# Kernel tuning notes

Hardware: AMD Instinct MI355X
Metric: run time of the kernel (lower is better)

Reference implementation:

```python
import jax, jax.numpy as jnp
import numpy as np

E, K, CAP = 6, 2, 192
ALPHA, LOAD_PEN, MIN_USE, TEMP = 0.7, 2.0, 0.05, 1.0
BN_EPS = 1e-5
NEG = -1e30


def conv3x3(x, w, b=None):
    y = jax.lax.conv_general_dilated(x, w, (1, 1), 'SAME',
                                     dimension_numbers=('NCHW', 'OIHW', 'NCHW'))
    if b is not None:
        y = y + b[None, :, None, None]
    return y


def bn_eval(x, g, b):
    # fresh BatchNorm buffers: running_mean=0, running_var=1
    s = g / jnp.sqrt(1.0 + BN_EPS)
    return x * s[None, :, None, None] + b[None, :, None, None]


def maxpool2(x):
    return jax.lax.reduce_window(x, -jnp.inf, jax.lax.max,
                                 (1, 1, 2, 2), (1, 1, 2, 2), 'VALID')


def avgpool_to2(x):
    B, C, H, W = x.shape
    return x.reshape(B, C, 2, H // 2, 2, W // 2).mean(axis=(3, 5))


def expert_forward(p, x):
    h = jax.nn.relu(bn_eval(conv3x3(x, p['c1w'], p['c1b']), p['b1g'], p['b1b']))
    h = maxpool2(h)  # 32 -> 16
    h = jax.nn.relu(bn_eval(conv3x3(h, p['c2w'], p['c2b']), p['b2g'], p['b2b']))
    h = jax.nn.relu(bn_eval(conv3x3(h, p['c3w'], p['c3b']), p['b3g'], p['b3b']))
    h = maxpool2(h)  # 16 -> 8
    h = jax.nn.relu(bn_eval(conv3x3(h, p['c4w'], p['c4b']), p['b4g'], p['b4b']))
    h = jax.nn.relu(bn_eval(conv3x3(h, p['c5w'], p['c5b']), p['b5g'], p['b5b']))
    feat = h.mean(axis=(2, 3))                       # global avg pool -> [B, c3]
    f = jax.nn.relu(feat @ p['fw'].T + p['fb'])      # [B, feat_dim]
    return f @ p['cw'].T + p['cb']                   # [B, num_classes]


def moe_forward(x, t_c1w, t_b1g, t_b1b, t_c2w, t_b2g, t_b2b, t_fcw, t_fcb,
                g1w, g1b, g2w, g2b,
                e_c1w, e_c1b, e_b1g, e_b1b, e_c2w, e_c2b, e_b2g, e_b2b,
                e_c3w, e_c3b, e_b3g, e_b3b, e_c4w, e_c4b, e_b4g, e_b4b,
                e_c5w, e_c5b, e_b5g, e_b5b, e_fw, e_fb, e_cw, e_cb, ema):
    B = x.shape[0]
    # --- routing trunk ---
    h = jax.nn.relu(bn_eval(conv3x3(x, t_c1w), t_b1g, t_b1b))
    h = jax.nn.relu(bn_eval(conv3x3(h, t_c2w), t_b2g, t_b2b))
    h = avgpool_to2(maxpool2(h)).reshape(B, -1)      # [B, 128]
    rf = jax.nn.relu(h @ t_fcw.T + t_fcb)            # [B, routing_dim]
    # --- gate (eval: no dropout, no noise) ---
    g = jax.nn.relu(rf @ g1w.T + g1b)
    gate_scores = (g @ g2w.T + g2b) / TEMP           # [B, E]
    # --- all experts on full batch (dense, as in source) ---
    ep = {'c1w': e_c1w, 'c1b': e_c1b, 'b1g': e_b1g, 'b1b': e_b1b,
          'c2w': e_c2w, 'c2b': e_c2b, 'b2g': e_b2g, 'b2b': e_b2b,
          'c3w': e_c3w, 'c3b': e_c3b, 'b3g': e_b3g, 'b3b': e_b3b,
          'c4w': e_c4w, 'c4b': e_c4b, 'b4g': e_b4g, 'b4b': e_b4b,
          'c5w': e_c5w, 'c5b': e_c5b, 'b5g': e_b5g, 'b5b': e_b5b,
          'fw': e_fw, 'fb': e_fb, 'cw': e_cw, 'cb': e_cb}
    logits_e = jax.vmap(expert_forward, in_axes=(0, None))(ep, x)  # [E, B, C]
    logits_e = jnp.transpose(logits_e, (1, 0, 2))                   # [B, E, C]
    # confidence = -entropy = sum p*log(p)
    logp = jax.nn.log_softmax(logits_e, axis=2)
    conf = (jnp.exp(logp) * jnp.log(jnp.exp(logp) + 1e-12)).sum(axis=2)  # [B, E]
    # --- balanced scores ---
    combined = ALPHA * gate_scores + (1.0 - ALPHA) * conf
    boost = jnp.where(ema < MIN_USE, (MIN_USE - ema) * 10.0, 0.0)
    combined = combined + boost[None, :]
    balanced = combined - LOAD_PEN * ema[None, :]
    # --- greedy capacity-constrained dispatch (deterministic order, eval) ---
    _, topk_idx = jax.lax.top_k(balanced, K)          # [B, K]

    def step(loads, idxs):
        l = loads[idxs]                                # [K]
        fits = l < CAP
        first = jnp.argmax(fits)                       # first expert with room
        fallback = idxs[jnp.argmin(l)]
        chosen = jnp.where(fits.any(), idxs[first], fallback)
        return loads.at[chosen].add(1.0), chosen

    _, chosen = jax.lax.scan(step, jnp.zeros((E,), balanced.dtype), topk_idx)
    D = jax.nn.one_hot(chosen, E, dtype=bool)          # [B, E]
    # --- weighted combine ---
    masked = jnp.where(D, balanced, NEG)
    w = jax.nn.softmax(masked, axis=1) * D.astype(balanced.dtype)
    w = w / (w.sum(axis=1, keepdims=True) + 1e-12)
    logits_final = (w[:, :, None] * logits_e).sum(axis=1)  # [B, C]
    return logits_final, balanced, D


def _params(key):
    ks = iter(jax.random.split(key, 64))
    rd, rd2, fd, nc, c1, c2, c3 = 64, 32, 128, 10, 32, 64, 128

    def w(shape, fan):
        return jax.random.normal(next(ks), shape, jnp.float32) * np.sqrt(2.0 / fan)

    p = {}
    p['t_c1w'] = w((32, 3, 3, 3), 32 * 9); p['t_b1g'] = jnp.ones(32); p['t_b1b'] = jnp.zeros(32)
    p['t_c2w'] = w((32, 32, 3, 3), 32 * 9); p['t_b2g'] = jnp.ones(32); p['t_b2b'] = jnp.zeros(32)
    p['t_fcw'] = w((rd, 128), rd); p['t_fcb'] = jnp.zeros(rd)
    p['g1w'] = w((rd2, rd), rd2); p['g1b'] = jnp.zeros(rd2)
    p['g2w'] = w((E, rd2), E); p['g2b'] = jnp.zeros(E)
    for i, (ci, co) in enumerate([(3, c1), (c1, c2), (c2, c2), (c2, c3), (c3, c3)], 1):
        p[f'e_c{i}w'] = w((E, co, ci, 3, 3), co * 9)
        p[f'e_c{i}b'] = jnp.zeros((E, co))
        p[f'e_b{i}g'] = jnp.ones((E, co))
        p[f'e_b{i}b'] = jnp.zeros((E, co))
    p['e_fw'] = w((E, fd, c3), fd); p['e_fb'] = jnp.zeros((E, fd))
    p['e_cw'] = w((E, nc, fd), nc); p['e_cb'] = jnp.zeros((E, nc))
    p['ema'] = jnp.ones((E,), jnp.float32) / E
    return p


def setup_inputs() -> dict:
    key = jax.random.key(0)
    kx, kp = jax.random.split(key)
    inp = {'x': jax.random.normal(kx, (1024, 3, 32, 32), jnp.float32)}
    inp.update(_params(kp))
    return inp


def reference(x, t_c1w, t_b1g, t_b1b, t_c2w, t_b2g, t_b2b, t_fcw, t_fcb,
              g1w, g1b, g2w, g2b,
              e_c1w, e_c1b, e_b1g, e_b1b, e_c2w, e_c2b, e_b2g, e_b2b,
              e_c3w, e_c3b, e_b3g, e_b3b, e_c4w, e_c4b, e_b4g, e_b4b,
              e_c5w, e_c5b, e_b5g, e_b5b, e_fw, e_fb, e_cw, e_cb, ema):
    return moe_forward(x, t_c1w, t_b1g, t_b1b, t_c2w, t_b2g, t_b2b, t_fcw, t_fcb,
                       g1w, g1b, g2w, g2b,
                       e_c1w, e_c1b, e_b1g, e_b1b, e_c2w, e_c2b, e_b2g, e_b2b,
                       e_c3w, e_c3b, e_b3g, e_b3b, e_c4w, e_c4b, e_b4g, e_b4b,
                       e_c5w, e_c5b, e_b5g, e_b5b, e_fw, e_fb, e_cw, e_cb, ema)
```

## Files before the change

### kernel.cpp

```cpp
#include <hip/hip_runtime.h>
#include <math.h>

#define B_ 1024
#define E_ 6

typedef _Float16 half8 __attribute__((ext_vector_type(8)));
typedef float f32x4 __attribute__((ext_vector_type(4)));

__device__ __forceinline__ unsigned short h_bits(_Float16 h) {
    union { _Float16 f; unsigned short u; } c; c.f = h; return c.u;
}
__device__ __forceinline__ unsigned int splitpack(float v) {
    _Float16 h = (_Float16)v;
    _Float16 l = (_Float16)((v - (float)h) * 2048.0f);
    return (unsigned int)h_bits(h) | ((unsigned int)h_bits(l) << 16);
}

__global__ void prep_w(const float* __restrict__ w, const float* __restrict__ g,
                       float* __restrict__ wout, int CO, int CI, int total) {
    int i = blockIdx.x * 256 + threadIdx.x;
    if (i >= total) return;
    int k = i % 9;
    int t = i / 9;
    int ci = t % CI; t /= CI;
    int co = t % CO;
    int e  = t / CO;
    float s = g[e * CO + co] * (1.0f / sqrtf(1.0f + 1e-5f));
    wout[(((long)(e * CI + ci) * 9 + k) * CO) + co] = w[i] * s;
}

__global__ void prep_b(const float* __restrict__ cb, const float* __restrict__ g,
                       const float* __restrict__ bb, float* __restrict__ bout, int N) {
    int i = blockIdx.x * 256 + threadIdx.x;
    if (i >= N) return;
    float s = g[i] * (1.0f / sqrtf(1.0f + 1e-5f));
    float c = (cb != nullptr) ? cb[i] : 0.0f;
    bout[i] = c * s + bb[i];
}

__global__ void prep_wfrag(const float* __restrict__ w, const float* __restrict__ g,
                           _Float16* __restrict__ out, int CI, int CO, int total) {
    int i = blockIdx.x * 256 + threadIdx.x;
    if (i >= total) return;
    const int NC = CI / 32;
    const int NB = CO / 16;
    int j = i & 7;
    int lane = (i >> 3) & 63;
    int rest = i >> 9;
    int chunk = rest % NC; rest /= NC;
    int tap = rest % 9; rest /= 9;
    int nbg = rest % NB;
    int e = rest / NB;
    int co = nbg * 16 + (lane & 15);
    int ci = chunk * 32 + ((lane >> 4) * 8) + j;
    float s = g[e * CO + co] * (1.0f / sqrtf(1.0f + 1e-5f));
    float v = w[(((long)(e * CO + co) * CI + ci) * 9) + tap] * s;
    _Float16 hi = (_Float16)v;
    _Float16 lo = (_Float16)((v - (float)hi) * 2048.0f);
    long perE = (long)NB * 9 * NC * 2 * 512;
    long F0 = ((long)(nbg * 9 + tap) * NC + chunk) * 2;
    long base = (long)e * perE + F0 * 512 + lane * 8 + j;
    out[base] = hi;
    out[base + 512] = lo;
}

template <int CI, int CO, int H, int TS, int CO_BLK, int CI_CHUNK, bool POOL, int OUTMODE>
__launch_bounds__(256)
__global__ void conv3x3(const float* __restrict__ in, const float* __restrict__ wt,
                        const float* __restrict__ bias, void* __restrict__ outv) {
    constexpr int TD = H / TS;
    constexpr int TILES = TD * TD;
    constexpr int LW = TS + 2;
    constexpr int NPX = POOL ? (TS / 2) * (TS / 2) : TS * TS;
    constexpr int G = 256 / NPX;
    constexpr int NG = CO / CO_BLK;
    constexpr int GPT = NG / G;
    constexpr int COT = GPT * CO_BLK;
    constexpr int NW = POOL ? 4 : 1;
    constexpr int OD = POOL ? TS / 2 : TS;

    __shared__ float lds[CI_CHUNK * LW * LW];

    int bid = blockIdx.x;
    int n = bid / TILES;
    int t = bid % TILES;
    int ty = (t / TD) * TS;
    int tx = (t % TD) * TS;
    int tid = threadIdx.x;
    int px = tid % NPX;
    int cg0 = tid / NPX;
    const int cg0s = __builtin_amdgcn_readfirstlane(cg0);
    int oy = px / OD;
    int ox = px % OD;

    float acc[NW][COT];
#pragma unroll
    for (int g2 = 0; g2 < GPT; ++g2)
#pragma unroll
        for (int j = 0; j < CO_BLK; ++j) {
            float bv = bias[(cg0s + g2 * G) * CO_BLK + j];
#pragma unroll
            for (int p = 0; p < NW; ++p) acc[p][g2 * CO_BLK + j] = bv;
        }

    for (int cc = 0; cc < CI / CI_CHUNK; ++cc) {
        const float* inb = in + ((long)n * CI + cc * CI_CHUNK) * (H * H);
        for (int idx = tid; idx < CI_CHUNK * LW * LW; idx += 256) {
            int ci = idx / (LW * LW);
            int r = idx - ci * (LW * LW);
            int yy = r / LW + ty - 1;
            int xx = r % LW + tx - 1;
            float v = 0.0f;
            if ((unsigned)yy < (unsigned)H && (unsigned)xx < (unsigned)H)
                v = inb[ci * H * H + yy * H + xx];
            lds[idx] = v;
        }
        __syncthreads();

        const float* wbase = wt + ((long)cc * CI_CHUNK) * 9 * CO;
        for (int ci = 0; ci < CI_CHUNK; ++ci) {
#pragma unroll
            for (int ky = 0; ky < 3; ++ky) {
#pragma unroll
                for (int kx = 0; kx < 3; ++kx) {
                    float v[NW];
                    if constexpr (POOL) {
#pragma unroll
                        for (int dy = 0; dy < 2; ++dy)
#pragma unroll
                            for (int dx = 0; dx < 2; ++dx)
                                v[dy * 2 + dx] =
                                    lds[ci * LW * LW + (2 * oy + dy + ky) * LW + (2 * ox + dx + kx)];
                    } else {
                        v[0] = lds[ci * LW * LW + (oy + ky) * LW + (ox + kx)];
                    }
                    const float* wr = wbase + ((ci * 3 + ky) * 3 + kx) * CO + cg0s * CO_BLK;
#pragma unroll
                    for (int g2 = 0; g2 < GPT; ++g2)
#pragma unroll
                        for (int j = 0; j < CO_BLK; ++j) {
                            float wv = wr[g2 * G * CO_BLK + j];
#pragma unroll
                            for (int p = 0; p < NW; ++p)
                                acc[p][g2 * CO_BLK + j] = fmaf(v[p], wv, acc[p][g2 * CO_BLK + j]);
                        }
                }
            }
        }
        __syncthreads();
    }

    if constexpr (OUTMODE == 1) {
        unsigned int* po = (unsigned int*)outv;
        long base;
        if constexpr (POOL) {
            constexpr int HP = H / 2;
            int pp = (ty / 2 + oy) * HP + (tx / 2 + ox);
            base = ((long)n * (HP * HP) + pp) * CO;
        } else {
            int pp = (ty + oy) * H + (tx + ox);
            base = ((long)n * (H * H) + pp) * CO;
        }
#pragma unroll
        for (int g2 = 0; g2 < GPT; ++g2) {
            int cobase = (cg0s + g2 * G) * CO_BLK;
#pragma unroll
            for (int j4 = 0; j4 < CO_BLK; j4 += 4) {
                uint4 u;
                unsigned int* up = (unsigned int*)&u;
#pragma unroll
                for (int jj = 0; jj < 4; ++jj) {
                    int a = g2 * CO_BLK + j4 + jj;
                    float v;
                    if constexpr (POOL)
                        v = fmaxf(fmaxf(acc[0][a], acc[1][a]), fmaxf(acc[2][a], acc[3][a]));
                    else
                        v = acc[0][a];
                    up[jj] = splitpack(fmaxf(v, 0.0f));
                }
                *(uint4*)(po + base + cobase + j4) = u;
            }
        }
    } else {
        float* out = (float*)outv;
        if constexpr (POOL) {
            constexpr int HP = H / 2;
            int py = ty / 2 + oy;
            int pxx = tx / 2 + ox;
#pragma unroll
            for (int g2 = 0; g2 < GPT; ++g2)
#pragma unroll
                for (int j = 0; j < CO_BLK; ++j) {
                    int co = (cg0s + g2 * G) * CO_BLK + j;
                    int a = g2 * CO_BLK + j;
                    float m = fmaxf(fmaxf(acc[0][a], acc[1][a]), fmaxf(acc[2][a], acc[3][a]));
                    out[((long)n * CO + co) * (HP * HP) + py * HP + pxx] = fmaxf(m, 0.0f);
                }
        } else {
            int yy = ty + oy;
            int xx = tx + ox;
#pragma unroll
            for (int g2 = 0; g2 < GPT; ++g2)
#pragma unroll
                for (int j = 0; j < CO_BLK; ++j) {
                    int co = (cg0s + g2 * G) * CO_BLK + j;
                    out[((long)n * CO + co) * (H * H) + yy * H + xx] =
                        fmaxf(acc[0][g2 * CO_BLK + j], 0.0f);
                }
        }
    }
}

__launch_bounds__(256, 2)
__global__ void conv_mfma_t2(const unsigned int* __restrict__ in,
                             const _Float16* __restrict__ wt,
                             const float* __restrict__ bias,
                             float* __restrict__ rf, int n0) {
    constexpr int PXS = 40;
    __shared__ _Float16 ldsH[18 * 18 * PXS];
    __shared__ _Float16 ldsL[18 * 18 * PXS];
    __shared__ float red[4][32];

    const int tid = threadIdx.x;
    const int wv = tid >> 6, lane = tid & 63;
    const int q = lane >> 4, l15 = lane & 15;
    const int bid = blockIdx.x;
    const int nl = bid >> 2, tile = bid & 3;
    const int ty2 = (tile >> 1) * 16, tx2 = (tile & 1) * 16;

    f32x4 accH[8], accL[8];
#pragma unroll
    for (int i = 0; i < 8; ++i) { accH[i] = (f32x4){0,0,0,0}; accL[i] = (f32x4){0,0,0,0}; }

    for (int u = tid; u < 18 * 18 * 8; u += 256) {
        int cu = u & 7;
        int p = u >> 3;
        int wy = p / 18, wx = p % 18;
        int gy = ty2 + wy - 1, gx = tx2 + wx - 1;
        uint4 w = make_uint4(0, 0, 0, 0);
        if ((unsigned)gy < 32u && (unsigned)gx < 32u)
            w = *(const uint4*)(in + ((long)nl * 1024 + gy * 32 + gx) * 32 + cu * 4);
        unsigned int h01 = (w.x & 0xffffu) | (w.y << 16);
        unsigned int h23 = (w.z & 0xffffu) | (w.w << 16);
        unsigned int l01 = (w.x >> 16) | (w.y & 0xffff0000u);
        unsigned int l23 = (w.z >> 16) | (w.w & 0xffff0000u);
        int fi = (wy * 18 + wx) * PXS + cu * 4;
        *(uint2*)(&ldsH[fi]) = make_uint2(h01, h23);
        *(uint2*)(&ldsL[fi]) = make_uint2(l01, l23);
    }
    __syncthreads();

#pragma unroll
    for (int ky = 0; ky < 3; ++ky)
#pragma unroll
        for (int kx = 0; kx < 3; ++kx) {
            const int tap = ky * 3 + kx;
            half8 ah[4], al[4];
#pragma unroll
            for (int mb = 0; mb < 4; ++mb) {
                int y = wv * 4 + mb;
                int fi = ((y + ky) * 18 + (l15 + kx)) * PXS + q * 8;
                ah[mb] = *(const half8*)&ldsH[fi];
                al[mb] = *(const half8*)&ldsL[fi];
            }
            half8 bh[2], bl[2];
#pragma unroll
            for (int nb = 0; nb < 2; ++nb) {
                int F0 = (nb * 9 + tap) * 2;
                bh[nb] = ((const half8*)wt)[(long)F0 * 64 + lane];
                bl[nb] = ((const half8*)wt)[(long)(F0 + 1) * 64 + lane];
            }
#pragma unroll
            for (int nb = 0; nb < 2; ++nb)
#pragma unroll
                for (int mb = 0; mb < 4; ++mb)
                    accH[mb * 2 + nb] = __builtin_amdgcn_mfma_f32_16x16x32_f16(
                        ah[mb], bh[nb], accH[mb * 2 + nb], 0, 0, 0);
#pragma unroll
            for (int nb = 0; nb < 2; ++nb)
#pragma unroll
                for (int mb = 0; mb < 4; ++mb)
                    accL[mb * 2 + nb] = __builtin_amdgcn_mfma_f32_16x16x32_f16(
                        ah[mb], bl[nb], accL[mb * 2 + nb], 0, 0, 0);
#pragma unroll
            for (int nb = 0; nb < 2; ++nb)
#pragma unroll
                for (int mb = 0; mb < 4; ++mb)
                    accL[mb * 2 + nb] = __builtin_amdgcn_mfma_f32_16x16x32_f16(
                        al[mb], bh[nb], accL[mb * 2 + nb], 0, 0, 0);
        }

    const float inv2048 = 1.0f / 2048.0f;
    float bv[2];
#pragma unroll
    for (int nb = 0; nb < 2; ++nb) bv[nb] = bias[nb * 16 + l15];
    float avg[2] = {0.0f, 0.0f};
#pragma unroll
    for (int k = 0; k < 2; ++k)
#pragma unroll
        for (int j = 0; j < 2; ++j)
#pragma unroll
            for (int nb = 0; nb < 2; ++nb) {
                float m = -1e30f;
#pragma unroll
                for (int dm = 0; dm < 2; ++dm)
#pragma unroll
                    for (int dr = 0; dr < 2; ++dr) {
                        int a = (2 * k + dm) * 2 + nb;
                        int r = 2 * j + dr;
                        float v = accH[a][r] + accL[a][r] * inv2048 + bv[nb];
                        m = fmaxf(m, v);
                    }
                avg[nb] += fmaxf(m, 0.0f);
            }
#pragma unroll
    for (int nb = 0; nb < 2; ++nb) {
        avg[nb] += __shfl_xor(avg[nb], 16);
        avg[nb] += __shfl_xor(avg[nb], 32);
    }
    if (q == 0) {
        red[wv][l15] = avg[0];
        red[wv][16 + l15] = avg[1];
    }
    __syncthreads();
    if (tid < 32) {
        float s = red[0][tid] + red[1][tid] + red[2][tid] + red[3][tid];
        int n = n0 + nl;
        rf[(long)n * 128 + tid * 4 + (tile >> 1) * 2 + (tile & 1)] = s * (1.0f / 64.0f);
    }
}

template <int CI, bool POOL>
__launch_bounds__(256, 2)
__global__ void conv_mfma16(const unsigned int* __restrict__ in,
                            const _Float16* __restrict__ wt,
                            const float* __restrict__ bias,
                            unsigned int* __restrict__ outp) {
    constexpr int NC = CI / 32;
    constexpr int PXS = 40;
    __shared__ _Float16 ldsH[18 * 18 * PXS];
    __shared__ _Float16 ldsL[18 * 18 * PXS];

    const int tid = threadIdx.x;
    const int wv = tid >> 6, lane = tid & 63;
    const int q = lane >> 4, l15 = lane & 15;
    const int n = blockIdx.x;

    {
        half8 z = {};
        half8* zh = (half8*)ldsH;
        half8* zl = (half8*)ldsL;
        for (int i = tid; i < 18 * 18 * PXS / 8; i += 256) { zh[i] = z; zl[i] = z; }
    }

    f32x4 accH[16], accL[16];
#pragma unroll
    for (int i = 0; i < 16; ++i) { accH[i] = (f32x4){0,0,0,0}; accL[i] = (f32x4){0,0,0,0}; }

    for (int c = 0; c < NC; ++c) {
        __syncthreads();
        for (int v = tid; v < 2048; v += 256) {
            int cu = v & 7;
            int px = v >> 3;
            long gidx = ((long)n * 256 + px) * CI + c * 32 + cu * 4;
            uint4 w = *(const uint4*)(in + gidx);
            unsigned int h01 = (w.x & 0xffffu) | (w.y << 16);
            unsigned int h23 = (w.z & 0xffffu) | (w.w << 16);
            unsigned int l01 = (w.x >> 16) | (w.y & 0xffff0000u);
            unsigned int l23 = (w.z >> 16) | (w.w & 0xffff0000u);
            int py = px >> 4, pxx = px & 15;
            int fi = ((py + 1) * 18 + (pxx + 1)) * PXS + cu * 4;
            *(uint2*)(&ldsH[fi]) = make_uint2(h01, h23);
            *(uint2*)(&ldsL[fi]) = make_uint2(l01, l23);
        }
        __syncthreads();

#pragma unroll
        for (int ky = 0; ky < 3; ++ky)
#pragma unroll
            for (int kx = 0; kx < 3; ++kx) {
                const int tap = ky * 3 + kx;
                half8 ah[4], al[4];
#pragma unroll
                for (int mb = 0; mb < 4; ++mb) {
                    int y = wv * 4 + mb;
                    int fi = ((y + ky) * 18 + (l15 + kx)) * PXS + q * 8;
                    ah[mb] = *(const half8*)&ldsH[fi];
                    al[mb] = *(const half8*)&ldsL[fi];
                }
                half8 bh[4], bl[4];
#pragma unroll
                for (int nb = 0; nb < 4; ++nb) {
                    int F0 = ((nb * 9 + tap) * NC + c) * 2;
                    bh[nb] = ((const half8*)wt)[(long)F0 * 64 + lane];
                    bl[nb] = ((const half8*)wt)[(long)(F0 + 1) * 64 + lane];
                }
#pragma unroll
                for (int nb = 0; nb < 4; ++nb)
#pragma unroll
                    for (int mb = 0; mb < 4; ++mb)
                        accH[mb * 4 + nb] = __builtin_amdgcn_mfma_f32_16x16x32_f16(
                            ah[mb], bh[nb], accH[mb * 4 + nb], 0, 0, 0);
#pragma unroll
                for (int nb = 0; nb < 4; ++nb)
#pragma unroll
                    for (int mb = 0; mb < 4; ++mb)
                        accL[mb * 4 + nb] = __builtin_amdgcn_mfma_f32_16x16x32_f16(
                            ah[mb], bl[nb], accL[mb * 4 + nb], 0, 0, 0);
#pragma unroll
                for (int nb = 0; nb < 4; ++nb)
#pragma unroll
                    for (int mb = 0; mb < 4; ++mb)
                        accL[mb * 4 + nb] = __builtin_amdgcn_mfma_f32_16x16x32_f16(
                            al[mb], bh[nb], accL[mb * 4 + nb], 0, 0, 0);
            }
    }

    const float inv2048 = 1.0f / 2048.0f;
    float bv[4];
#pragma unroll
    for (int nb = 0; nb < 4; ++nb) bv[nb] = bias[nb * 16 + l15];

    if constexpr (POOL) {
#pragma unroll
        for (int k = 0; k < 2; ++k) {
#pragma unroll
            for (int j = 0; j < 2; ++j) {
                int yy = wv * 2 + k;
                int xx = q * 2 + j;
                long base = ((long)n * 64 + yy * 8 + xx) * 64;
#pragma unroll
                for (int nb = 0; nb < 4; ++nb) {
                    float m = -1e30f;
#pragma unroll
                    for (int dm = 0; dm < 2; ++dm)
#pragma unroll
                        for (int dr = 0; dr < 2; ++dr) {
                            int a = (2 * k + dm) * 4 + nb;
                            int r = 2 * j + dr;
                            float v = accH[a][r] + accL[a][r] * inv2048 + bv[nb];
                            m = fmaxf(m, v);
                        }
                    m = fmaxf(m, 0.0f);
                    outp[base + nb * 16 + l15] = splitpack(m);
                }
            }
        }
    } else {
#pragma unroll
        for (int mb = 0; mb < 4; ++mb) {
            int y = wv * 4 + mb;
#pragma unroll
            for (int r = 0; r < 4; ++r) {
                int px = y * 16 + q * 4 + r;
                long base = ((long)n * 256 + px) * 64;
#pragma unroll
                for (int nb = 0; nb < 4; ++nb) {
                    float v = accH[mb * 4 + nb][r] + accL[mb * 4 + nb][r] * inv2048 + bv[nb];
                    v = fmaxf(v, 0.0f);
                    outp[base + nb * 16 + l15] = splitpack(v);
                }
            }
        }
    }
}

__launch_bounds__(256, 2)
__global__ void conv_c345(const unsigned int* __restrict__ in,
                          const _Float16* __restrict__ wt3, const float* __restrict__ b3,
                          const _Float16* __restrict__ wt4, const float* __restrict__ b4,
                          const _Float16* __restrict__ wt5, const float* __restrict__ b5,
                          float* __restrict__ feat) {
    __shared__ _Float16 poolA[25920];
    __shared__ _Float16 poolB[12800];
    _Float16* AH = poolA;
    _Float16* AL = poolA + 12960;
    _Float16* CH = poolA;
    _Float16* CL = poolA + 12800;
    _Float16* BH = poolB;
    _Float16* BL = poolB + 6400;

    const int tid = threadIdx.x;
    const int wv = tid >> 6, lane = tid & 63;
    const int q = lane >> 4, l15 = lane & 15;
    const int n = blockIdx.x;
    const float inv2048 = 1.0f / 2048.0f;

    {
        half8 z = {};
        half8* za = (half8*)poolA;
        for (int i = tid; i < 3240; i += 256) za[i] = z;
        half8* zb = (half8*)poolB;
        for (int i = tid; i < 1600; i += 256) zb[i] = z;
    }

    f32x4 accH[16], accL[16];
#pragma unroll
    for (int i = 0; i < 16; ++i) { accH[i] = (f32x4){0,0,0,0}; accL[i] = (f32x4){0,0,0,0}; }

    for (int c = 0; c < 2; ++c) {
        __syncthreads();
        for (int v = tid; v < 2048; v += 256) {
            int cu = v & 7;
            int px = v >> 3;
            long gidx = ((long)n * 256 + px) * 64 + c * 32 + cu * 4;
            uint4 w = *(const uint4*)(in + gidx);
            unsigned int h01 = (w.x & 0xffffu) | (w.y << 16);
            unsigned int h23 = (w.z & 0xffffu) | (w.w << 16);
            unsigned int l01 = (w.x >> 16) | (w.y & 0xffff0000u);
            unsigned int l23 = (w.z >> 16) | (w.w & 0xffff0000u);
            int py = px >> 4, pxx = px & 15;
            int fi = ((py + 1) * 18 + (pxx + 1)) * 40 + cu * 4;
            *(uint2*)(&AH[fi]) = make_uint2(h01, h23);
            *(uint2*)(&AL[fi]) = make_uint2(l01, l23);
        }
        __syncthreads();

#pragma unroll
        for (int ky = 0; ky < 3; ++ky)
#pragma unroll
            for (int kx = 0; kx < 3; ++kx) {
                const int tap = ky * 3 + kx;
                half8 ah[4], al[4];
#pragma unroll
                for (int mb = 0; mb < 4; ++mb) {
                    int y = wv * 4 + mb;
                    int fi = ((y + ky) * 18 + (l15 + kx)) * 40 + q * 8;
                    ah[mb] = *(const half8*)&AH[fi];
                    al[mb] = *(const half8*)&AL[fi];
                }
                half8 bh[4], bl[4];
#pragma unroll
                for (int nb = 0; nb < 4; ++nb) {
                    int F0 = ((nb * 9 + tap) * 2 + c) * 2;
                    bh[nb] = ((const half8*)wt3)[(long)F0 * 64 + lane];
                    bl[nb] = ((const half8*)wt3)[(long)(F0 + 1) * 64 + lane];
                }
#pragma unroll
                for (int nb = 0; nb < 4; ++nb)
#pragma unroll
                    for (int mb = 0; mb < 4; ++mb)
                        accH[mb * 4 + nb] = __builtin_amdgcn_mfma_f32_16x16x32_f16(
                            ah[mb], bh[nb], accH[mb * 4 + nb], 0, 0, 0);
#pragma unroll
                for (int nb = 0; nb < 4; ++nb)
#pragma unroll
                    for (int mb = 0; mb < 4; ++mb)
                        accL[mb * 4 + nb] = __builtin_amdgcn_mfma_f32_16x16x32_f16(
                            ah[mb], bl[nb], accL[mb * 4 + nb], 0, 0, 0);
#pragma unroll
                for (int nb = 0; nb < 4; ++nb)
#pragma unroll
                    for (int mb = 0; mb < 4; ++mb)
                        accL[mb * 4 + nb] = __builtin_amdgcn_mfma_f32_16x16x32_f16(
                            al[mb], bh[nb], accL[mb * 4 + nb], 0, 0, 0);
            }
    }
    __syncthreads();

    {
        half8 z = {};
        half8* za = (half8*)poolA;
        for (int i = tid; i < 3240; i += 256) za[i] = z;
    }
    {
        float bv[4];
#pragma unroll
        for (int nb = 0; nb < 4; ++nb) bv[nb] = b3[nb * 16 + l15];
#pragma unroll
        for (int k = 0; k < 2; ++k)
#pragma unroll
            for (int j = 0; j < 2; ++j) {
                int yy = wv * 2 + k;
                int xx = q * 2 + j;
                int p = (yy + 1) * 10 + (xx + 1);
#pragma unroll
                for (int nb = 0; nb < 4; ++nb) {
                    float m = -1e30f;
#pragma unroll
                    for (int dm = 0; dm < 2; ++dm)
#pragma unroll
                        for (int dr = 0; dr < 2; ++dr) {
                            int a = (2 * k + dm) * 4 + nb;
                            int r = 2 * j + dr;
                            float v = accH[a][r] + accL[a][r] * inv2048 + bv[nb];
                            m = fmaxf(m, v);
                        }
                    m = fmaxf(m, 0.0f);
                    _Float16 hi = (_Float16)m;
                    _Float16 lo = (_Float16)((m - (float)hi) * 2048.0f);
                    int ci = nb * 16 + l15;
                    int bi = (ci >> 5) * 3200 + p * 32 + (ci & 31);
                    BH[bi] = hi;
                    BL[bi] = lo;
                }
            }
    }
    __syncthreads();

#pragma unroll
    for (int i = 0; i < 8; ++i) { accH[i] = (f32x4){0,0,0,0}; accL[i] = (f32x4){0,0,0,0}; }

    for (int c = 0; c < 2; ++c) {
#pragma unroll
        for (int ky = 0; ky < 3; ++ky)
#pragma unroll
            for (int kx = 0; kx < 3; ++kx) {
                const int tap = ky * 3 + kx;
                half8 ah[4], al[4];
#pragma unroll
                for (int mb = 0; mb < 4; ++mb) {
                    int m = mb * 16 + l15;
                    int fi = c * 3200 + (((m >> 3) + ky) * 10 + ((m & 7) + kx)) * 32 + q * 8;
                    ah[mb] = *(const half8*)&BH[fi];
                    al[mb] = *(const half8*)&BL[fi];
                }
                half8 bh[2], bl[2];
#pragma unroll
                for (int nb = 0; nb < 2; ++nb) {
                    int nbg = wv * 2 + nb;
                    int F0 = ((nbg * 9 + tap) * 2 + c) * 2;
                    bh[nb] = ((const half8*)wt4)[(long)F0 * 64 + lane];
                    bl[nb] = ((const half8*)wt4)[(long)(F0 + 1) * 64 + lane];
                }
#pragma unroll
                for (int nb = 0; nb < 2; ++nb)
#pragma unroll
                    for (int mb = 0; mb < 4; ++mb)
                        accH[mb * 2 + nb] = __builtin_amdgcn_mfma_f32_16x16x32_f16(
                            ah[mb], bh[nb], accH[mb * 2 + nb], 0, 0, 0);
#pragma unroll
                for (int nb = 0; nb < 2; ++nb)
#pragma unroll
                    for (int mb = 0; mb < 4; ++mb)
                        accL[mb * 2 + nb] = __builtin_amdgcn_mfma_f32_16x16x32_f16(
                            ah[mb], bl[nb], accL[mb * 2 + nb], 0, 0, 0);
#pragma unroll
                for (int nb = 0; nb < 2; ++nb)
#pragma unroll
                    for (int mb = 0; mb < 4; ++mb)
                        accL[mb * 2 + nb] = __builtin_amdgcn_mfma_f32_16x16x32_f16(
                            al[mb], bh[nb], accL[mb * 2 + nb], 0, 0, 0);
            }
    }

    {
        float bv[2];
#pragma unroll
        for (int nb = 0; nb < 2; ++nb) bv[nb] = b4[wv * 32 + nb * 16 + l15];
#pragma unroll
        for (int mb = 0; mb < 4; ++mb)
#pragma unroll
            for (int r = 0; r < 4; ++r) {
                int px = mb * 16 + q * 4 + r;
                int p = ((px >> 3) + 1) * 10 + ((px & 7) + 1);
#pragma unroll
                for (int nb = 0; nb < 2; ++nb) {
                    float v = accH[mb * 2 + nb][r] + accL[mb * 2 + nb][r] * inv2048 + bv[nb];
                    v = fmaxf(v, 0.0f);
                    _Float16 hi = (_Float16)v;
                    _Float16 lo = (_Float16)((v - (float)hi) * 2048.0f);
                    int ci = nb * 16 + l15;
                    CH[wv * 3200 + p * 32 + ci] = hi;
                    CL[wv * 3200 + p * 32 + ci] = lo;
                }
            }
    }
    __syncthreads();

#pragma unroll
    for (int i = 0; i < 8; ++i) { accH[i] = (f32x4){0,0,0,0}; accL[i] = (f32x4){0,0,0,0}; }

    for (int c = 0; c < 4; ++c) {
#pragma unroll
        for (int ky = 0; ky < 3; ++ky)
#pragma unroll
            for (int kx = 0; kx < 3; ++kx) {
                const int tap = ky * 3 + kx;
                half8 ah[4], al[4];
#pragma unroll
                for (int mb = 0; mb < 4; ++mb) {
                    int m = mb * 16 + l15;
                    int fi = c * 3200 + (((m >> 3) + ky) * 10 + ((m & 7) + kx)) * 32 + q * 8;
                    ah[mb] = *(const half8*)&CH[fi];
                    al[mb] = *(const half8*)&CL[fi];
                }
                half8 bh[2], bl[2];
#pragma unroll
                for (int nb = 0; nb < 2; ++nb) {
                    int nbg = wv * 2 + nb;
                    int F0 = ((nbg * 9 + tap) * 4 + c) * 2;
                    bh[nb] = ((const half8*)wt5)[(long)F0 * 64 + lane];
                    bl[nb] = ((const half8*)wt5)[(long)(F0 + 1) * 64 + lane];
                }
#pragma unroll
                for (int nb = 0; nb < 2; ++nb)
#pragma unroll
                    for (int mb = 0; mb < 4; ++mb)
                        accH[mb * 2 + nb] = __builtin_amdgcn_mfma_f32_16x16x32_f16(
                            ah[mb], bh[nb], accH[mb * 2 + nb], 0, 0, 0);
#pragma unroll
                for (int nb = 0; nb < 2; ++nb)
#pragma unroll
                    for (int mb = 0; mb < 4; ++mb)
                        accL[mb * 2 + nb] = __builtin_amdgcn_mfma_f32_16x16x32_f16(
                            ah[mb], bl[nb], accL[mb * 2 + nb], 0, 0, 0);
#pragma unroll
                for (int nb = 0; nb < 2; ++nb)
#pragma unroll
                    for (int mb = 0; mb < 4; ++mb)
                        accL[mb * 2 + nb] = __builtin_amdgcn_mfma_f32_16x16x32_f16(
                            al[mb], bh[nb], accL[mb * 2 + nb], 0, 0, 0);
            }
    }

    {
        float bv[2];
#pragma unroll
        for (int nb = 0; nb < 2; ++nb) bv[nb] = b5[wv * 32 + nb * 16 + l15];
        float s0 = 0.0f, s1 = 0.0f;
#pragma unroll
        for (int mb = 0; mb < 4; ++mb)
#pragma unroll
            for (int r = 0; r < 4; ++r) {
                float v0 = accH[mb * 2 + 0][r] + accL[mb * 2 + 0][r] * inv2048 + bv[0];
                float v1 = accH[mb * 2 + 1][r] + accL[mb * 2 + 1][r] * inv2048 + bv[1];
                s0 += fmaxf(v0, 0.0f);
                s1 += fmaxf(v1, 0.0f);
            }
        s0 += __shfl_xor(s0, 16); s0 += __shfl_xor(s0, 32);
        s1 += __shfl_xor(s1, 16); s1 += __shfl_xor(s1, 32);
        if (lane < 16) {
            long fb_ = (long)n * 128 + wv * 32 + l15;
            feat[fb_] = s0 * (1.0f / 64.0f);
            feat[fb_ + 16] = s1 * (1.0f / 64.0f);
        }
    }
}

__launch_bounds__(128)
__global__ void head_k(const float* __restrict__ feat, const float* __restrict__ fw,
                       const float* __restrict__ fb, const float* __restrict__ cw,
                       const float* __restrict__ cb, float* __restrict__ outl) {
    __shared__ float fe[128];
    __shared__ float fv[128];
    int n = blockIdx.x, t = threadIdx.x;
    fe[t] = feat[(long)n * 128 + t];
    __syncthreads();
    const float* wr = fw + t * 128;
    float a = fb[t];
#pragma unroll 8
    for (int k = 0; k < 128; ++k) a = fmaf(fe[k], wr[k], a);
    fv[t] = fmaxf(a, 0.0f);
    __syncthreads();
    if (t < 10) {
        const float* cr = cw + t * 128;
        float a2 = cb[t];
#pragma unroll 8
        for (int k = 0; k < 128; ++k) a2 = fmaf(fv[k], cr[k], a2);
        outl[n * 10 + t] = a2;
    }
}

template <int I, int O, bool RELU>
__global__ void fc_k(const float* __restrict__ in, const float* __restrict__ W,
                     const float* __restrict__ bias, float* __restrict__ out) {
    int g = blockIdx.x * 256 + threadIdx.x;
    if (g >= B_ * O) return;
    int n = g / O;
    int o = g - n * O;
    const float* ip = in + (long)n * I;
    const float* wp = W + (long)o * I;
    float a = bias[o];
#pragma unroll 8
    for (int k = 0; k < I; ++k) a = fmaf(ip[k], wp[k], a);
    if (RELU) a = fmaxf(a, 0.0f);
    out[g] = a;
}

__global__ void conf_bal_k(const float* __restrict__ logitsE, const float* __restrict__ gate,
                           const float* __restrict__ ema, float* __restrict__ balanced,
                           unsigned char* __restrict__ cand) {
    int b = blockIdx.x * 256 + threadIdx.x;
    if (b >= B_) return;
    float bal[E_];
#pragma unroll
    for (int e = 0; e < E_; ++e) {
        const float* lp = logitsE + ((long)e * B_ + b) * 10;
        float m = lp[0];
#pragma unroll
        for (int k = 1; k < 10; ++k) m = fmaxf(m, lp[k]);
        float s = 0.0f;
#pragma unroll
        for (int k = 0; k < 10; ++k) s += expf(lp[k] - m);
        float ls = m + logf(s);
        float conf = 0.0f;
#pragma unroll
        for (int k = 0; k < 10; ++k) {
            float pp = expf(lp[k] - ls);
            conf += pp * logf(pp + 1e-12f);
        }
        float em = ema[e];
        float boost = (em < 0.05f) ? (0.05f - em) * 10.0f : 0.0f;
        bal[e] = 0.7f * gate[b * E_ + e] + 0.3f * conf + boost - 2.0f * em;
        balanced[b * E_ + e] = bal[e];
    }
    int i0 = 0;
    float m0 = bal[0];
#pragma unroll
    for (int e = 1; e < E_; ++e)
        if (bal[e] > m0) { m0 = bal[e]; i0 = e; }
    int i1 = -1;
    float m1 = -1e38f;
#pragma unroll
    for (int e = 0; e < E_; ++e)
        if (e != i0 && bal[e] > m1) { m1 = bal[e]; i1 = e; }
    cand[b] = (unsigned char)(i0 | (i1 << 3));
}

__global__ void dispatch_k(const unsigned char* __restrict__ cand, int* __restrict__ chosen) {
    int lane = threadIdx.x;
    unsigned long long L = 0;
    for (int r = 0; r < 16; ++r) {
        unsigned int v = cand[r * 64 + lane];
        int ch = 0;
        for (int q2 = 0; q2 < 64; ++q2) {
            unsigned int s = (unsigned int)__builtin_amdgcn_readlane((int)v, q2);
            unsigned int i0 = s & 7u;
            unsigned int i1 = (s >> 3) & 7u;
            unsigned int a0 = (unsigned int)(L >> (i0 * 10)) & 1023u;
            unsigned int a1 = (unsigned int)(L >> (i1 * 10)) & 1023u;
            unsigned int fb = (a1 < a0) ? i1 : i0;
            unsigned int c = (a0 < 192u) ? i0 : ((a1 < 192u) ? i1 : fb);
            if (lane == q2) ch = (int)c;
            L += 1ull << (c * 10);
        }
        chosen[r * 64 + lane] = ch;
    }
}

__global__ void final_k(const float* __restrict__ logitsE, const int* __restrict__ chosen,
                        float* __restrict__ out) {
    int b = blockIdx.x * 256 + threadIdx.x;
    if (b >= B_) return;
    int c = chosen[b];
    const float w = 1.0f / (1.0f + 1e-12f);
    const float* lp = logitsE + ((long)c * B_ + b) * 10;
#pragma unroll
    for (int k = 0; k < 10; ++k) out[b * 10 + k] = lp[k] * w;
    float* Dp = out + B_ * 10 + B_ * E_ + b * E_;
#pragma unroll
    for (int e = 0; e < E_; ++e) Dp[e] = (e == c) ? 1.0f : 0.0f;
}

extern "C" void kernel_launch(void* const* d_in, const int* in_sizes, int n_in,
                              void* d_out, int out_size, void* d_ws, size_t ws_size,
                              hipStream_t stream) {
    (void)in_sizes; (void)n_in; (void)out_size; (void)ws_size;
    const float* x     = (const float*)d_in[0];
    const float* t_c1w = (const float*)d_in[1];
    const float* t_b1g = (const float*)d_in[2];
    const float* t_b1b = (const float*)d_in[3];
    const float* t_c2w = (const float*)d_in[4];
    const float* t_b2g = (const float*)d_in[5];
    const float* t_b2b = (const float*)d_in[6];
    const float* t_fcw = (const float*)d_in[7];
    const float* t_fcb = (const float*)d_in[8];
    const float* g1w   = (const float*)d_in[9];
    const float* g1b   = (const float*)d_in[10];
    const float* g2w   = (const float*)d_in[11];
    const float* g2b   = (const float*)d_in[12];
    const float* e_c1w = (const float*)d_in[13];
    const float* e_c1b = (const float*)d_in[14];
    const float* e_b1g = (const float*)d_in[15];
    const float* e_b1b = (const float*)d_in[16];
    const float* e_c2w = (const float*)d_in[17];
    const float* e_c2b = (const float*)d_in[18];
    const float* e_b2g = (const float*)d_in[19];
    const float* e_b2b = (const float*)d_in[20];
    const float* e_c3w = (const float*)d_in[21];
    const float* e_c3b = (const float*)d_in[22];
    const float* e_b3g = (const float*)d_in[23];
    const float* e_b3b = (const float*)d_in[24];
    const float* e_c4w = (const float*)d_in[25];
    const float* e_c4b = (const float*)d_in[26];
    const float* e_b4g = (const float*)d_in[27];
    const float* e_b4b = (const float*)d_in[28];
    const float* e_c5w = (const float*)d_in[29];
    const float* e_c5b = (const float*)d_in[30];
    const float* e_b5g = (const float*)d_in[31];
    const float* e_b5b = (const float*)d_in[32];
    const float* e_fw  = (const float*)d_in[33];
    const float* e_fb  = (const float*)d_in[34];
    const float* e_cw  = (const float*)d_in[35];
    const float* e_cb  = (const float*)d_in[36];
    const float* ema   = (const float*)d_in[37];
    float* out = (float*)d_out;
    float* ws  = (float*)d_ws;

    size_t o = 0;
    float* R1f = ws + o; o += 8388608;
    float* R2f = ws + o; o += 16777216;
    float* rf_in   = ws + o; o += B_ * 128;
    float* rf      = ws + o; o += B_ * 64;
    float* gv      = ws + o; o += B_ * 32;
    float* gate    = ws + o; o += B_ * E_;
    float* logitsE = ws + o; o += E_ * B_ * 10;
    float* featb   = ws + o; o += B_ * 128;
    int*   chosen  = (int*)(ws + o); o += B_;
    unsigned char* cand = (unsigned char*)(ws + o); o += 256;
    float* wt_t1 = ws + o; o += 864;
    float* bt_t1 = ws + o; o += 32;
    float* bt_t2 = ws + o; o += 32;
    float* wt_c1 = ws + o; o += 6 * 864;
    float* bt_c1 = ws + o; o += 6 * 32;
    float* bt_c2 = ws + o; o += 6 * 64;
    float* bt_c3 = ws + o; o += 6 * 64;
    float* bt_c4 = ws + o; o += 6 * 128;
    float* bt_c5 = ws + o; o += 6 * 128;
    _Float16* wfrag_t2 = (_Float16*)(ws + o); o += 9216;
    _Float16* wfrag_c2 = (_Float16*)(ws + o); o += 110592;
    _Float16* wfrag_c3 = (_Float16*)(ws + o); o += 221184;
    _Float16* wfrag_c4 = (_Float16*)(ws + o); o += 442368;
    _Float16* wfrag_c5 = (_Float16*)(ws + o); o += 884736;

    unsigned int* R1u = (unsigned int*)R1f;
    unsigned int* R2u = (unsigned int*)R2f;

    auto gsz = [](int n) { return (n + 255) / 256; };
    prep_w<<<gsz(864), 256, 0, stream>>>(t_c1w, t_b1g, wt_t1, 32, 3, 864);
    prep_b<<<1, 256, 0, stream>>>(nullptr, t_b1g, t_b1b, bt_t1, 32);
    prep_wfrag<<<gsz(9216), 256, 0, stream>>>(t_c2w, t_b2g, wfrag_t2, 32, 32, 9216);
    prep_b<<<1, 256, 0, stream>>>(nullptr, t_b2g, t_b2b, bt_t2, 32);
    prep_w<<<gsz(5184), 256, 0, stream>>>(e_c1w, e_b1g, wt_c1, 32, 3, 5184);
    prep_b<<<1, 256, 0, stream>>>(e_c1b, e_b1g, e_b1b, bt_c1, 192);
    prep_wfrag<<<gsz(110592), 256, 0, stream>>>(e_c2w, e_b2g, wfrag_c2, 32, 64, 110592);
    prep_b<<<2, 256, 0, stream>>>(e_c2b, e_b2g, e_b2b, bt_c2, 384);
    prep_wfrag<<<gsz(221184), 256, 0, stream>>>(e_c3w, e_b3g, wfrag_c3, 64, 64, 221184);
    prep_b<<<2, 256, 0, stream>>>(e_c3b, e_b3g, e_b3b, bt_c3, 384);
    prep_wfrag<<<gsz(442368), 256, 0, stream>>>(e_c4w, e_b4g, wfrag_c4, 64, 128, 442368);
    prep_b<<<3, 256, 0, stream>>>(e_c4b, e_b4g, e_b4b, bt_c4, 768);
    prep_wfrag<<<gsz(884736), 256, 0, stream>>>(e_c5w, e_b5g, wfrag_c5, 128, 128, 884736);
    prep_b<<<3, 256, 0, stream>>>(e_c5b, e_b5g, e_b5b, bt_c5, 768);

    for (int q = 0; q < 2; ++q) {
        const float* xq = x + (size_t)q * 512 * 3 * 1024;
        conv3x3<3, 32, 32, 16, 32, 3, false, 1><<<512 * 4, 256, 0, stream>>>(
            xq, wt_t1, bt_t1, (void*)R2u);
        conv_mfma_t2<<<512 * 4, 256, 0, stream>>>(R2u, wfrag_t2, bt_t2, rf_in, q * 512);
    }
    fc_k<128, 64, true><<<256, 256, 0, stream>>>(rf_in, t_fcw, t_fcb, rf);
    fc_k<64, 32, true><<<128, 256, 0, stream>>>(rf, g1w, g1b, gv);
    fc_k<32, 6, false><<<24, 256, 0, stream>>>(gv, g2w, g2b, gate);

    for (int e = 0; e < E_; ++e) {
        conv3x3<3, 32, 32, 16, 8, 3, true, 1><<<B_ * 4, 256, 0, stream>>>(
            x, wt_c1 + e * 864, bt_c1 + e * 32, (void*)R1u);
        conv_mfma16<32, false><<<B_, 256, 0, stream>>>(
            R1u, wfrag_c2 + (size_t)e * 36864, bt_c2 + e * 64, R2u);
        conv_c345<<<B_, 256, 0, stream>>>(
            R2u, wfrag_c3 + (size_t)e * 73728, bt_c3 + e * 64,
            wfrag_c4 + (size_t)e * 147456, bt_c4 + e * 128,
            wfrag_c5 + (size_t)e * 294912, bt_c5 + e * 128, featb);
        head_k<<<B_, 128, 0, stream>>>(featb, e_fw + e * 16384, e_fb + e * 128,
                                       e_cw + e * 1280, e_cb + e * 10,
                                       logitsE + (size_t)e * B_ * 10);
    }

    float* balanced = out + B_ * 10;
    conf_bal_k<<<4, 256, 0, stream>>>(logitsE, gate, ema, balanced, cand);
    dispatch_k<<<1, 64, 0, stream>>>(cand, chosen);
    final_k<<<4, 256, 0, stream>>>(logitsE, chosen, out);
}
```

Before: 1.577 ms.

## Fuse expert conv1+pool into conv2 kernel and swizzle LDS in conv_c345

Replaces the separate conv1 (with maxpool) kernel and the templated conv2 MFMA kernel with one fused kernel per image. Conv1 is computed in FP32 from an LDS-staged padded input, pooled, and written straight into the split-half LDS tiles that conv2 consumes. This removes the global round trip of the intermediate activation and one launch per expert. Separately, it adds an XOR bank swizzle to the LDS tile indexing in conv_c345 to reduce bank conflicts. The fused kernel uses more LDS (input, weights and both half tiles), which may lower occupancy, and conv1 now runs on only 256 threads per image.

```diff
diff --git a/kernel.cpp b/kernel.cpp
--- a/kernel.cpp
+++ b/kernel.cpp
@@ -15,6 +15,7 @@
     _Float16 l = (_Float16)((v - (float)h) * 2048.0f);
     return (unsigned int)h_bits(h) | ((unsigned int)h_bits(l) << 16);
 }
+__device__ __forceinline__ int bswz(int fi, int p) { return fi ^ (((p >> 1) & 3) << 3); }
 
 __global__ void prep_w(const float* __restrict__ w, const float* __restrict__ g,
                        float* __restrict__ wout, int CO, int CI, int total) {
@@ -330,16 +331,16 @@
     }
 }
 
-template <int CI, bool POOL>
 __launch_bounds__(256, 2)
-__global__ void conv_mfma16(const unsigned int* __restrict__ in,
-                            const _Float16* __restrict__ wt,
-                            const float* __restrict__ bias,
-                            unsigned int* __restrict__ outp) {
-    constexpr int NC = CI / 32;
-    constexpr int PXS = 40;
-    __shared__ _Float16 ldsH[18 * 18 * PXS];
-    __shared__ _Float16 ldsL[18 * 18 * PXS];
+__global__ void conv_c12(const float* __restrict__ x,
+                         const float* __restrict__ w1, const float* __restrict__ b1,
+                         const _Float16* __restrict__ wt2, const float* __restrict__ b2,
+                         unsigned int* __restrict__ outp) {
+    __shared__ float xs[3 * 1156];
+    __shared__ float w1s[864];
+    __shared__ float b1s[32];
+    __shared__ _Float16 ldsH[18 * 18 * 40];
+    __shared__ _Float16 ldsL[18 * 18 * 40];
 
     const int tid = threadIdx.x;
     const int wv = tid >> 6, lane = tid & 63;
@@ -350,116 +351,131 @@
         half8 z = {};
         half8* zh = (half8*)ldsH;
         half8* zl = (half8*)ldsL;
-        for (int i = tid; i < 18 * 18 * PXS / 8; i += 256) { zh[i] = z; zl[i] = z; }
-    }
+        for (int i = tid; i < 18 * 18 * 40 / 8; i += 256) { zh[i] = z; zl[i] = z; }
+    }
+    for (int i = tid; i < 864; i += 256) w1s[i] = w1[i];
+    if (tid < 32) b1s[tid] = b1[tid];
+    for (int i = tid; i < 3 * 1156; i += 256) {
+        int c = i / 1156;
+        int r = i - c * 1156;
+        int yy = r / 34 - 1, xx = r % 34 - 1;
+        float v = 0.0f;
+        if ((unsigned)yy < 32u && (unsigned)xx < 32u)
+            v = x[((long)n * 3 + c) * 1024 + yy * 32 + xx];
+        xs[i] = v;
+    }
+    __syncthreads();
+
+    {
+        const int py = tid >> 4, px = tid & 15;
+#pragma unroll
+        for (int cog = 0; cog < 4; ++cog) {
+            float a[4][8];
+#pragma unroll
+            for (int j = 0; j < 8; ++j) {
+                float bv = b1s[cog * 8 + j];
+#pragma unroll
+                for (int p = 0; p < 4; ++p) a[p][j] = bv;
+            }
+            for (int ci = 0; ci < 3; ++ci) {
+                float patch[16];
+#pragma unroll
+                for (int r = 0; r < 4; ++r)
+#pragma unroll
+                    for (int cpx = 0; cpx < 4; ++cpx)
+                        patch[r * 4 + cpx] = xs[ci * 1156 + (2 * py + r) * 34 + (2 * px + cpx)];
+#pragma unroll
+                for (int ky = 0; ky < 3; ++ky)
+#pragma unroll
+                    for (int kx = 0; kx < 3; ++kx) {
+                        const float* wr = &w1s[((ci * 3 + ky) * 3 + kx) * 32 + cog * 8];
+#pragma unroll
+                        for (int j = 0; j < 8; ++j) {
+                            float wvv = wr[j];
+#pragma unroll
+                            for (int dy = 0; dy < 2; ++dy)
+#pragma unroll
+                                for (int dx = 0; dx < 2; ++dx)
+                                    a[dy * 2 + dx][j] =
+                                        fmaf(patch[(dy + ky) * 4 + (dx + kx)], wvv,
+                                             a[dy * 2 + dx][j]);
+                        }
+                    }
+            }
+            int fibase = ((py + 1) * 18 + (px + 1)) * 40 + cog * 8;
+#pragma unroll
+            for (int j = 0; j < 8; ++j) {
+                float m = fmaxf(fmaxf(a[0][j], a[1][j]), fmaxf(a[2][j], a[3][j]));
+                m = fmaxf(m, 0.0f);
+                _Float16 hi = (_Float16)m;
+                _Float16 lo = (_Float16)((m - (float)hi) * 2048.0f);
+                ldsH[fibase + j] = hi;
+                ldsL[fibase + j] = lo;
+            }
+        }
+    }
+    __syncthreads();
 
     f32x4 accH[16], accL[16];
 #pragma unroll
     for (int i = 0; i < 16; ++i) { accH[i] = (f32x4){0,0,0,0}; accL[i] = (f32x4){0,0,0,0}; }
 
-    for (int c = 0; c < NC; ++c) {
-        __syncthreads();
-        for (int v = tid; v < 2048; v += 256) {
-            int cu = v & 7;
-            int px = v >> 3;
-            long gidx = ((long)n * 256 + px) * CI + c * 32 + cu * 4;
-            uint4 w = *(const uint4*)(in + gidx);
-            unsigned int h01 = (w.x & 0xffffu) | (w.y << 16);
-            unsigned int h23 = (w.z & 0xffffu) | (w.w << 16);
-            unsigned int l01 = (w.x >> 16) | (w.y & 0xffff0000u);
-            unsigned int l23 = (w.z >> 16) | (w.w & 0xffff0000u);
-            int py = px >> 4, pxx = px & 15;
-            int fi = ((py + 1) * 18 + (pxx + 1)) * PXS + cu * 4;
-            *(uint2*)(&ldsH[fi]) = make_uint2(h01, h23);
-            *(uint2*)(&ldsL[fi]) = make_uint2(l01, l23);
-        }
-        __syncthreads();
-
-#pragma unroll
-        for (int ky = 0; ky < 3; ++ky)
-#pragma unroll
-            for (int kx = 0; kx < 3; ++kx) {
-                const int tap = ky * 3 + kx;
-                half8 ah[4], al[4];
-#pragma unroll
-                for (int mb = 0; mb < 4; ++mb) {
-                    int y = wv * 4 + mb;
-                    int fi = ((y + ky) * 18 + (l15 + kx)) * PXS + q * 8;
-                    ah[mb] = *(const half8*)&ldsH[fi];
-                    al[mb] = *(const half8*)&ldsL[fi];
-                }
-                half8 bh[4], bl[4];
-#pragma unroll
-                for (int nb = 0; nb < 4; ++nb) {
-                    int F0 = ((nb * 9 + tap) * NC + c) * 2;
-                    bh[nb] = ((const half8*)wt)[(long)F0 * 64 + lane];
-                    bl[nb] = ((const half8*)wt)[(long)(F0 + 1) * 64 + lane];
-                }
-#pragma unroll
-                for (int nb = 0; nb < 4; ++nb)
-#pragma unroll
-                    for (int mb = 0; mb < 4; ++mb)
-                        accH[mb * 4 + nb] = __builtin_amdgcn_mfma_f32_16x16x32_f16(
-                            ah[mb], bh[nb], accH[mb * 4 + nb], 0, 0, 0);
-#pragma unroll
-                for (int nb = 0; nb < 4; ++nb)
-#pragma unroll
-                    for (int mb = 0; mb < 4; ++mb)
-                        accL[mb * 4 + nb] = __builtin_amdgcn_mfma_f32_16x16x32_f16(
-                            ah[mb], bl[nb], accL[mb * 4 + nb], 0, 0, 0);
-#pragma unroll
-                for (int nb = 0; nb < 4; ++nb)
-#pragma unroll
-                    for (int mb = 0; mb < 4; ++mb)
-                        accL[mb * 4 + nb] = __builtin_amdgcn_mfma_f32_16x16x32_f16(
-                            al[mb], bh[nb], accL[mb * 4 + nb], 0, 0, 0);
-            }
-    }
+#pragma unroll
+    for (int ky = 0; ky < 3; ++ky)
+#pragma unroll
+        for (int kx = 0; kx < 3; ++kx) {
+            const int tap = ky * 3 + kx;
+            half8 ah[4], al[4];
+#pragma unroll
+            for (int mb = 0; mb < 4; ++mb) {
+                int y = wv * 4 + mb;
+                int fi = ((y + ky) * 18 + (l15 + kx)) * 40 + q * 8;
+                ah[mb] = *(const half8*)&ldsH[fi];
+                al[mb] = *(const half8*)&ldsL[fi];
+            }
+            half8 bh[4], bl[4];
+#pragma unroll
+            for (int nb = 0; nb < 4; ++nb) {
+                int F0 = (nb * 9 + tap) * 2;
+                bh[nb] = ((const half8*)wt2)[(long)F0 * 64 + lane];
+                bl[nb] = ((const half8*)wt2)[(long)(F0 + 1) * 64 + lane];
+            }
+#pragma unroll
+            for (int nb = 0; nb < 4; ++nb)
+#pragma unroll
+                for (int mb = 0; mb < 4; ++mb)
+                    accH[mb * 4 + nb] = __builtin_amdgcn_mfma_f32_16x16x32_f16(
+                        ah[mb], bh[nb], accH[mb * 4 + nb], 0, 0, 0);
+#pragma unroll
+            for (int nb = 0; nb < 4; ++nb)
+#pragma unroll
+                for (int mb = 0; mb < 4; ++mb)
+                    accL[mb * 4 + nb] = __builtin_amdgcn_mfma_f32_16x16x32_f16(
+                        ah[mb], bl[nb], accL[mb * 4 + nb], 0, 0, 0);
+#pragma unroll
+            for (int nb = 0; nb < 4; ++nb)
+#pragma unroll
+                for (int mb = 0; mb < 4; ++mb)
+                    accL[mb * 4 + nb] = __builtin_amdgcn_mfma_f32_16x16x32_f16(
+                        al[mb], bh[nb], accL[mb * 4 + nb], 0, 0, 0);
+        }
 
     const float inv2048 = 1.0f / 2048.0f;
     float bv[4];
 #pragma unroll
-    for (int nb = 0; nb < 4; ++nb) bv[nb] = bias[nb * 16 + l15];
-
-    if constexpr (POOL) {
-#pragma unroll
-        for (int k = 0; k < 2; ++k) {
-#pragma unroll
-            for (int j = 0; j < 2; ++j) {
-                int yy = wv * 2 + k;
-                int xx = q * 2 + j;
-                long base = ((long)n * 64 + yy * 8 + xx) * 64;
-#pragma unroll
-                for (int nb = 0; nb < 4; ++nb) {
-                    float m = -1e30f;
-#pragma unroll
-                    for (int dm = 0; dm < 2; ++dm)
-#pragma unroll
-                        for (int dr = 0; dr < 2; ++dr) {
-                            int a = (2 * k + dm) * 4 + nb;
-                            int r = 2 * j + dr;
-                            float v = accH[a][r] + accL[a][r] * inv2048 + bv[nb];
-                            m = fmaxf(m, v);
-                        }
-                    m = fmaxf(m, 0.0f);
-                    outp[base + nb * 16 + l15] = splitpack(m);
-                }
-            }
-        }
-    } else {
-#pragma unroll
-        for (int mb = 0; mb < 4; ++mb) {
-            int y = wv * 4 + mb;
-#pragma unroll
-            for (int r = 0; r < 4; ++r) {
-                int px = y * 16 + q * 4 + r;
-                long base = ((long)n * 256 + px) * 64;
-#pragma unroll
-                for (int nb = 0; nb < 4; ++nb) {
-                    float v = accH[mb * 4 + nb][r] + accL[mb * 4 + nb][r] * inv2048 + bv[nb];
-                    v = fmaxf(v, 0.0f);
-                    outp[base + nb * 16 + l15] = splitpack(v);
-                }
+    for (int nb = 0; nb < 4; ++nb) bv[nb] = b2[nb * 16 + l15];
+#pragma unroll
+    for (int mb = 0; mb < 4; ++mb) {
+        int y = wv * 4 + mb;
+#pragma unroll
+        for (int r = 0; r < 4; ++r) {
+            int px = y * 16 + q * 4 + r;
+            long base = ((long)n * 256 + px) * 64;
+#pragma unroll
+            for (int nb = 0; nb < 4; ++nb) {
+                float v = accH[mb * 4 + nb][r] + accL[mb * 4 + nb][r] * inv2048 + bv[nb];
+                v = fmaxf(v, 0.0f);
+                outp[base + nb * 16 + l15] = splitpack(v);
             }
         }
     }
@@ -590,7 +606,7 @@
                     _Float16 hi = (_Float16)m;
                     _Float16 lo = (_Float16)((m - (float)hi) * 2048.0f);
                     int ci = nb * 16 + l15;
-                    int bi = (ci >> 5) * 3200 + p * 32 + (ci & 31);
+                    int bi = bswz((ci >> 5) * 3200 + p * 32 + (ci & 31), p);
                     BH[bi] = hi;
                     BL[bi] = lo;
                 }
@@ -611,7 +627,8 @@
 #pragma unroll
                 for (int mb = 0; mb < 4; ++mb) {
                     int m = mb * 16 + l15;
-                    int fi = c * 3200 + (((m >> 3) + ky) * 10 + ((m & 7) + kx)) * 32 + q * 8;
+                    int p = ((m >> 3) + ky) * 10 + ((m & 7) + kx);
+                    int fi = bswz(c * 3200 + p * 32 + q * 8, p);
                     ah[mb] = *(const half8*)&BH[fi];
                     al[mb] = *(const half8*)&BL[fi];
                 }
@@ -661,8 +678,9 @@
                     _Float16 hi = (_Float16)v;
                     _Float16 lo = (_Float16)((v - (float)hi) * 2048.0f);
                     int ci = nb * 16 + l15;
-                    CH[wv * 3200 + p * 32 + ci] = hi;
-                    CL[wv * 3200 + p * 32 + ci] = lo;
+                    int fi = bswz(wv * 3200 + p * 32 + ci, p);
+                    CH[fi] = hi;
+                    CL[fi] = lo;
                 }
             }
     }
@@ -681,7 +699,8 @@
 #pragma unroll
                 for (int mb = 0; mb < 4; ++mb) {
                     int m = mb * 16 + l15;
-                    int fi = c * 3200 + (((m >> 3) + ky) * 10 + ((m & 7) + kx)) * 32 + q * 8;
+                    int p = ((m >> 3) + ky) * 10 + ((m & 7) + kx);
+                    int fi = bswz(c * 3200 + p * 32 + q * 8, p);
                     ah[mb] = *(const half8*)&CH[fi];
                     al[mb] = *(const half8*)&CL[fi];
                 }
@@ -924,8 +943,8 @@
     _Float16* wfrag_c4 = (_Float16*)(ws + o); o += 442368;
     _Float16* wfrag_c5 = (_Float16*)(ws + o); o += 884736;
 
-    unsigned int* R1u = (unsigned int*)R1f;
     unsigned int* R2u = (unsigned int*)R2f;
+    (void)R1f;
 
     auto gsz = [](int n) { return (n + 255) / 256; };
     prep_w<<<gsz(864), 256, 0, stream>>>(t_c1w, t_b1g, wt_t1, 32, 3, 864);
@@ -954,10 +973,9 @@
     fc_k<32, 6, false><<<24, 256, 0, stream>>>(gv, g2w, g2b, gate);
 
     for (int e = 0; e < E_; ++e) {
-        conv3x3<3, 32, 32, 16, 8, 3, true, 1><<<B_ * 4, 256, 0, stream>>>(
-            x, wt_c1 + e * 864, bt_c1 + e * 32, (void*)R1u);
-        conv_mfma16<32, false><<<B_, 256, 0, stream>>>(
-            R1u, wfrag_c2 + (size_t)e * 36864, bt_c2 + e * 64, R2u);
+        conv_c12<<<B_, 256, 0, stream>>>(
+            x, wt_c1 + e * 864, bt_c1 + e * 32,
+            wfrag_c2 + (size_t)e * 36864, bt_c2 + e * 64, R2u);
         conv_c345<<<B_, 256, 0, stream>>>(
             R2u, wfrag_c3 + (size_t)e * 73728, bt_c3 + e * 64,
             wfrag_c4 + (size_t)e * 147456, bt_c4 + e * 128,
```

Measured after the change: 1.596 ms. About the same (+1.2%).
